# Performance work log

Measured on AMD Instinct MI355X. Metric: run time of the kernel, lower is better.

Reference implementation:

```python
import jax, jax.numpy as jnp
import numpy as np

N_TOKENS = 8192
NQ = 6
NL = 2


def ry_mat(theta):
    # theta: scalar or (B,) -> (2,2) or (B,2,2) complex RY matrix
    c = jnp.cos(theta / 2)
    s = jnp.sin(theta / 2)
    return jnp.stack([jnp.stack([c, -s], -1), jnp.stack([s, c], -1)], -2).astype(jnp.complex64)


def apply_1q(state, gate, q, nq):
    # state: (B, 2**nq); gate: (2,2) shared or (B,2,2) per-batch
    B = state.shape[0]
    st = state.reshape(B, 2 ** q, 2, -1)
    if gate.ndim == 3:
        st = jnp.einsum('bij,bajc->baic', gate, st)
    else:
        st = jnp.einsum('ij,bajc->baic', gate, st)
    return st.reshape(B, -1)


def apply_rz(state, theta, q, nq):
    # diagonal RZ: multiply phases, no matmul needed
    B = state.shape[0]
    st = state.reshape(B, 2 ** q, 2, -1)
    ph = jnp.stack([jnp.exp(-0.5j * theta), jnp.exp(0.5j * theta)]).astype(jnp.complex64)
    return (st * ph[None, None, :, None]).reshape(B, -1)


def apply_cnot(state, c, t, nq):
    B = state.shape[0]
    st = state.reshape((B,) + (2,) * nq)
    s0 = jnp.take(st, 0, axis=1 + c)
    s1 = jnp.take(st, 1, axis=1 + c)
    ta = 1 + t - (1 if t > c else 0)  # target axis after removing control axis
    s1 = jnp.flip(s1, axis=ta)
    st = jnp.stack([s0, s1], axis=1 + c)
    return st.reshape(B, -1)


def prepare_states(x, params, nl, nq):
    # x: (B, nq) angles; params: (nl, nq, 2). Returns (B, 2**nq) complex statevectors.
    B = x.shape[0]
    state = jnp.zeros((B, 2 ** nq), jnp.complex64).at[:, 0].set(1.0)
    for q in range(nq):  # RY angle embedding
        state = apply_1q(state, ry_mat(x[:, q]), q, nq)
    for l in range(nl):  # PQC layers: RY, RZ rotations + CNOT ring
        for q in range(nq):
            state = apply_1q(state, ry_mat(params[l, q, 0]), q, nq)
            state = apply_rz(state, params[l, q, 1], q, nq)
        for q in range(nq):
            state = apply_cnot(state, q, (q + 1) % nq, nq)
    return state


def setup_inputs() -> dict:
    key = jax.random.key(0)
    k1, k2, k3, k4 = jax.random.split(key, 4)
    return {
        'x_tokens': jax.random.normal(k1, (N_TOKENS, NQ), dtype=jnp.float32),
        'params_q': 0.1 * jax.random.normal(k2, (NL, NQ, 2), dtype=jnp.float32),
        'params_k': 0.1 * jax.random.normal(k3, (NL, NQ, 2), dtype=jnp.float32),
        'params_v': 0.1 * jax.random.normal(k4, (NL, NQ, 2), dtype=jnp.float32),
    }


def reference(x_tokens, params_q, params_k, params_v):
    nq = x_tokens.shape[1]
    nl = params_q.shape[0]
    sq = prepare_states(x_tokens, params_q, nl, nq)  # (N, 2**nq)
    sk = prepare_states(x_tokens, params_k, nl, nq)
    ov = jnp.einsum('id,jd->ij', sq, jnp.conj(sk))  # pairwise overlaps (N, N)
    logits = jnp.real(ov * jnp.conj(ov))            # swap-test fidelity |<q|k>|^2
    attn = jax.nn.softmax(logits, axis=-1)
    sv = prepare_states(x_tokens, params_v, nl, nq)
    probs = jnp.real(sv * jnp.conj(sv))             # (N, 2**nq)
    idx = jnp.arange(2 ** nq)
    bits = (idx[None, :] >> (nq - 1 - jnp.arange(nq))[:, None]) & 1  # (nq, 2**nq)
    signs = (1.0 - 2.0 * bits).astype(probs.dtype)
    V = probs @ signs.T                              # <Z_q> per qubit -> (N, nq)
    return attn @ V
```

## Files before the change

### kernel.cpp

```cpp
#include <hip/hip_runtime.h>
#include <hip/hip_bf16.h>

#define NT 8192
#define NQB 6
#define NL 2
#define JSPLIT 16
#define JSLICE (NT / JSPLIT)
#define CHUNK 64
#define NCHUNK (JSLICE / CHUNK)
#define IPW 32
#define WPB 4
#define IPB (IPW * WPB)
#define NBI (NT / IPB)

typedef __bf16 bf16x8 __attribute__((ext_vector_type(8)));
typedef float f32x4 __attribute__((ext_vector_type(4)));

static __device__ __forceinline__ unsigned int pack_bf2(float a, float b) {
  unsigned short lo = __builtin_bit_cast(unsigned short, __float2bfloat16(a));
  unsigned short hi = __builtin_bit_cast(unsigned short, __float2bfloat16(b));
  return (unsigned int)lo | ((unsigned int)hi << 16);
}

static __device__ __forceinline__ int cnot_src(int p, int q) {
  const int mc = 1 << (5 - q);
  const int mt = 1 << (5 - ((q + 1) % NQB));
  return (p & mc) ? (p ^ mt) : p;
}

__global__ __launch_bounds__(256) void prep_kernel(
    const float* __restrict__ x, const float* __restrict__ pq,
    const float* __restrict__ pk, const float* __restrict__ pv,
    unsigned int* __restrict__ Are, unsigned int* __restrict__ Bk,
    float4* __restrict__ V4)
{
  const int wid  = blockIdx.x * 4 + (threadIdx.x >> 6);
  const int lane = threadIdx.x & 63;
  const int set  = wid >> 13;
  const int tok  = wid & (NT - 1);
  const float* pp = (set == 0) ? pq : ((set == 1) ? pk : pv);

  int m = lane;
#pragma unroll
  for (int q = 5; q >= 0; --q) m = cnot_src(m, q);
  int inv = lane;
#pragma unroll
  for (int q = 0; q < 6; ++q) inv = cnot_src(inv, q);

  float R = 1.f, phi = 0.f;
#pragma unroll
  for (int q = 0; q < 6; ++q) {
    float s, c;
    __sincosf(0.5f * (x[tok * NQB + q] + pp[q * 2 + 0]), &s, &c);
    const float bh = 0.5f * pp[q * 2 + 1];
    if ((m >> (5 - q)) & 1) { R *= s; phi += bh; }
    else                    { R *= c; phi -= bh; }
  }
  float sp, cp;
  __sincosf(phi, &sp, &cp);
  float re = R * cp, im = R * sp;

#pragma unroll
  for (int q = 0; q < 6; ++q) {
    const int mask = 1 << (5 - q);
    float s, c;
    __sincosf(0.5f * pp[2 * NQB + q * 2 + 0], &s, &c);
    const float pre = __shfl_xor(re, mask, 64);
    const float pim = __shfl_xor(im, mask, 64);
    const float se = (lane & mask) ? s : -s;
    re = fmaf(se, pre, c * re);
    im = fmaf(se, pim, c * im);
  }
  float phi2 = 0.f;
#pragma unroll
  for (int q = 0; q < 6; ++q) {
    const float bh = 0.5f * pp[2 * NQB + q * 2 + 1];
    phi2 += (lane & (1 << (5 - q))) ? bh : -bh;
  }
  float s2, c2;
  __sincosf(phi2, &s2, &c2);
  const float fre = re * c2 - im * s2;
  const float fim = re * s2 + im * c2;

  if (set == 0) {
    Are[tok * 64 + inv] = pack_bf2(fre, fim);
  } else if (set == 1) {
    Bk[tok * 64 + inv] = pack_bf2(fre, fim);
  } else {
    const float prob = fre * fre + fim * fim;
    float vq[NQB];
#pragma unroll
    for (int q = 0; q < NQB; ++q) {
      float v = (inv & (1 << (5 - q))) ? -prob : prob;
#pragma unroll
      for (int off = 1; off < 64; off <<= 1) v += __shfl_xor(v, off, 64);
      vq[q] = v;
    }
    if (lane == 0) {
      V4[tok * 2 + 0] = make_float4(vq[0], vq[1], vq[2], vq[3]);
      V4[tok * 2 + 1] = make_float4(vq[4], vq[5], 0.f, 0.f);
    }
  }
}

__global__ __launch_bounds__(256, 2) void attn_kernel(
    const uint4* __restrict__ Are, const uint4* __restrict__ Bk,
    const float4* __restrict__ V4, float* __restrict__ part)
{
  __shared__ uint4 kbuf[CHUNK * 17];
  __shared__ float4 vbuf[CHUNK * 2];

  const int tid  = threadIdx.x;
  const int lane = tid & 63;
  const int wave = tid >> 6;
  const int col  = lane & 15;
  const int quad = lane >> 4;

  const int ib = blockIdx.x & (NBI - 1);
  const int js = blockIdx.x / NBI;
  const int ibase = ib * IPB + wave * IPW;
  const int jbase0 = js * JSLICE;

  bf16x8 aRe[2][4], aIm[2][4];
#pragma unroll
  for (int rt = 0; rt < 2; ++rt) {
    const int row = ibase + rt * 16 + col;
    const uint4* pr = Are + row * 16 + quad;
#pragma unroll
    for (int s = 0; s < 4; ++s) {
      const uint4 u = pr[s * 4];
      uint4 w;
      w.x = ((u.x << 16) | (u.x >> 16)) ^ 0x80000000u;
      w.y = ((u.y << 16) | (u.y >> 16)) ^ 0x80000000u;
      w.z = ((u.z << 16) | (u.z >> 16)) ^ 0x80000000u;
      w.w = ((u.w << 16) | (u.w >> 16)) ^ 0x80000000u;
      aRe[rt][s] = __builtin_bit_cast(bf16x8, u);
      aIm[rt][s] = __builtin_bit_cast(bf16x8, w);
    }
  }

  float den[8];
  float num[8][6];
#pragma unroll
  for (int r = 0; r < 8; ++r) {
    den[r] = 0.f;
#pragma unroll
    for (int q = 0; q < 6; ++q) num[r][q] = 0.f;
  }

#pragma unroll 1
  for (int c = 0; c < NCHUNK; ++c) {
    const int jb = jbase0 + c * CHUNK;
    __syncthreads();
#pragma unroll
    for (int r = 0; r < 4; ++r) {
      const int idx = r * 256 + tid;
      kbuf[(idx >> 4) * 17 + (idx & 15)] = Bk[(jb + (idx >> 4)) * 16 + (idx & 15)];
    }
    if (tid < 2 * CHUNK) vbuf[tid] = V4[jb * 2 + tid];
    __syncthreads();

#pragma unroll
    for (int ct = 0; ct < 4; ++ct) {
      const int keyl = ct * 16 + col;
      bf16x8 bfr[4];
#pragma unroll
      for (int s = 0; s < 4; ++s)
        bfr[s] = __builtin_bit_cast(bf16x8, kbuf[keyl * 17 + s * 4 + quad]);
      const float4 v01 = vbuf[keyl * 2 + 0];
      const float4 v23 = vbuf[keyl * 2 + 1];
      const float vv[6] = {v01.x, v01.y, v01.z, v01.w, v23.x, v23.y};
#pragma unroll
      for (int rt = 0; rt < 2; ++rt) {
        f32x4 aR = {0.f, 0.f, 0.f, 0.f};
        f32x4 aI = {0.f, 0.f, 0.f, 0.f};
#pragma unroll
        for (int s = 0; s < 4; ++s) {
          aR = __builtin_amdgcn_mfma_f32_16x16x32_bf16(aRe[rt][s], bfr[s], aR, 0, 0, 0);
          aI = __builtin_amdgcn_mfma_f32_16x16x32_bf16(aIm[rt][s], bfr[s], aI, 0, 0, 0);
        }
#pragma unroll
        for (int r = 0; r < 4; ++r) {
          const float f = aR[r] * aR[r] + aI[r] * aI[r];
          const float w = __expf(f);
          const int rr = rt * 4 + r;
          den[rr] += w;
#pragma unroll
          for (int q = 0; q < 6; ++q) num[rr][q] = fmaf(w, vv[q], num[rr][q]);
        }
      }
    }
  }

#pragma unroll
  for (int rr = 0; rr < 8; ++rr) {
#pragma unroll
    for (int off = 1; off < 16; off <<= 1) {
      den[rr] += __shfl_xor(den[rr], off, 64);
#pragma unroll
      for (int q = 0; q < 6; ++q) num[rr][q] += __shfl_xor(num[rr][q], off, 64);
    }
  }

  if (col == 0) {
#pragma unroll
    for (int rt = 0; rt < 2; ++rt) {
#pragma unroll
      for (int r = 0; r < 4; ++r) {
        const int row = ibase + rt * 16 + quad * 4 + r;
        float* p = part + ((size_t)(js * NT + row)) * 8;
        const int rr = rt * 4 + r;
#pragma unroll
        for (int q = 0; q < 6; ++q) p[q] = num[rr][q];
        p[6] = den[rr];
      }
    }
  }
}

__global__ __launch_bounds__(256) void combine_kernel(
    const float* __restrict__ part, float* __restrict__ out)
{
  const int row = blockIdx.x * 256 + threadIdx.x;
  float acc[7] = {0.f, 0.f, 0.f, 0.f, 0.f, 0.f, 0.f};
#pragma unroll
  for (int js = 0; js < JSPLIT; ++js) {
    const float* p = part + ((size_t)(js * NT + row)) * 8;
#pragma unroll
    for (int q = 0; q < 7; ++q) acc[q] += p[q];
  }
  const float inv = 1.0f / acc[6];
#pragma unroll
  for (int q = 0; q < 6; ++q)
    out[row * 6 + q] = acc[q] * inv;
}

extern "C" void kernel_launch(void* const* d_in, const int* in_sizes, int n_in,
                              void* d_out, int out_size, void* d_ws, size_t ws_size,
                              hipStream_t stream) {
  const float* x  = (const float*)d_in[0];
  const float* pq = (const float*)d_in[1];
  const float* pk = (const float*)d_in[2];
  const float* pv = (const float*)d_in[3];
  char* ws = (char*)d_ws;
  unsigned int* Are = (unsigned int*)(ws);
  unsigned int* Bk  = (unsigned int*)(ws + (size_t)(2u << 20));
  float*        V   = (float*)(ws + (size_t)(4u << 20));
  float*        prt = (float*)(ws + (size_t)(4u << 20) + (size_t)(256u << 10));

  prep_kernel<<<(NT * 3) / 4, 256, 0, stream>>>(x, pq, pk, pv, Are, Bk, (float4*)V);
  attn_kernel<<<NBI * JSPLIT, 256, 0, stream>>>((const uint4*)Are, (const uint4*)Bk,
                                                (const float4*)V, prt);
  combine_kernel<<<NT / 256, 256, 0, stream>>>(prt, (float*)d_out);
}
```

Measured before the change: 129.5 us.

## Load keys directly from global, preload V slice, restructure combine layout

The attention kernel no longer stages key chunks through shared memory with a barrier per chunk. Each wave now reads key fragments straight from global memory, relying on L1/L2 since all four waves share the same keys, and the whole V slice is preloaded once into LDS. The partial-results layout becomes row-major per js so the combine kernel can use coalesced float4 loads with 8 threads per row and a shuffle reduction. The prep kernel swaps __sincosf for separate __sinf/__cosf calls. Skipping the LDS staging risks redundant global traffic and exposed load latency in the MFMA loop.

```diff
diff --git a/kernel.cpp b/kernel.cpp
--- a/kernel.cpp
+++ b/kernel.cpp
@@ -6,12 +6,11 @@
 #define NL 2
 #define JSPLIT 16
 #define JSLICE (NT / JSPLIT)
-#define CHUNK 64
-#define NCHUNK (JSLICE / CHUNK)
 #define IPW 32
 #define WPB 4
 #define IPB (IPW * WPB)
 #define NBI (NT / IPB)
+#define NCT (JSLICE / 16)
 
 typedef __bf16 bf16x8 __attribute__((ext_vector_type(8)));
 typedef float f32x4 __attribute__((ext_vector_type(4)));
@@ -50,21 +49,19 @@
   float R = 1.f, phi = 0.f;
 #pragma unroll
   for (int q = 0; q < 6; ++q) {
-    float s, c;
-    __sincosf(0.5f * (x[tok * NQB + q] + pp[q * 2 + 0]), &s, &c);
+    const float t = 0.5f * (x[tok * NQB + q] + pp[q * 2 + 0]);
+    const float s = __sinf(t), c = __cosf(t);
     const float bh = 0.5f * pp[q * 2 + 1];
     if ((m >> (5 - q)) & 1) { R *= s; phi += bh; }
     else                    { R *= c; phi -= bh; }
   }
-  float sp, cp;
-  __sincosf(phi, &sp, &cp);
-  float re = R * cp, im = R * sp;
+  float re = R * __cosf(phi), im = R * __sinf(phi);
 
 #pragma unroll
   for (int q = 0; q < 6; ++q) {
     const int mask = 1 << (5 - q);
-    float s, c;
-    __sincosf(0.5f * pp[2 * NQB + q * 2 + 0], &s, &c);
+    const float t = 0.5f * pp[2 * NQB + q * 2 + 0];
+    const float s = __sinf(t), c = __cosf(t);
     const float pre = __shfl_xor(re, mask, 64);
     const float pim = __shfl_xor(im, mask, 64);
     const float se = (lane & mask) ? s : -s;
@@ -77,8 +74,7 @@
     const float bh = 0.5f * pp[2 * NQB + q * 2 + 1];
     phi2 += (lane & (1 << (5 - q))) ? bh : -bh;
   }
-  float s2, c2;
-  __sincosf(phi2, &s2, &c2);
+  const float s2 = __sinf(phi2), c2 = __cosf(phi2);
   const float fre = re * c2 - im * s2;
   const float fim = re * s2 + im * c2;
 
@@ -107,8 +103,7 @@
     const uint4* __restrict__ Are, const uint4* __restrict__ Bk,
     const float4* __restrict__ V4, float* __restrict__ part)
 {
-  __shared__ uint4 kbuf[CHUNK * 17];
-  __shared__ float4 vbuf[CHUNK * 2];
+  __shared__ float4 vbuf[JSLICE * 2];
 
   const int tid  = threadIdx.x;
   const int lane = tid & 63;
@@ -119,7 +114,11 @@
   const int ib = blockIdx.x & (NBI - 1);
   const int js = blockIdx.x / NBI;
   const int ibase = ib * IPB + wave * IPW;
-  const int jbase0 = js * JSLICE;
+  const int jbase = js * JSLICE;
+
+#pragma unroll
+  for (int r = 0; r < 4; ++r)
+    vbuf[r * 256 + tid] = V4[jbase * 2 + r * 256 + tid];
 
   bf16x8 aRe[2][4], aIm[2][4];
 #pragma unroll
@@ -148,46 +147,39 @@
     for (int q = 0; q < 6; ++q) num[r][q] = 0.f;
   }
 
-#pragma unroll 1
-  for (int c = 0; c < NCHUNK; ++c) {
-    const int jb = jbase0 + c * CHUNK;
-    __syncthreads();
-#pragma unroll
-    for (int r = 0; r < 4; ++r) {
-      const int idx = r * 256 + tid;
-      kbuf[(idx >> 4) * 17 + (idx & 15)] = Bk[(jb + (idx >> 4)) * 16 + (idx & 15)];
-    }
-    if (tid < 2 * CHUNK) vbuf[tid] = V4[jb * 2 + tid];
-    __syncthreads();
-
-#pragma unroll
-    for (int ct = 0; ct < 4; ++ct) {
-      const int keyl = ct * 16 + col;
-      bf16x8 bfr[4];
-#pragma unroll
-      for (int s = 0; s < 4; ++s)
-        bfr[s] = __builtin_bit_cast(bf16x8, kbuf[keyl * 17 + s * 4 + quad]);
-      const float4 v01 = vbuf[keyl * 2 + 0];
-      const float4 v23 = vbuf[keyl * 2 + 1];
-      const float vv[6] = {v01.x, v01.y, v01.z, v01.w, v23.x, v23.y};
-#pragma unroll
-      for (int rt = 0; rt < 2; ++rt) {
-        f32x4 aR = {0.f, 0.f, 0.f, 0.f};
-        f32x4 aI = {0.f, 0.f, 0.f, 0.f};
-#pragma unroll
-        for (int s = 0; s < 4; ++s) {
-          aR = __builtin_amdgcn_mfma_f32_16x16x32_bf16(aRe[rt][s], bfr[s], aR, 0, 0, 0);
-          aI = __builtin_amdgcn_mfma_f32_16x16x32_bf16(aIm[rt][s], bfr[s], aI, 0, 0, 0);
-        }
-#pragma unroll
-        for (int r = 0; r < 4; ++r) {
-          const float f = aR[r] * aR[r] + aI[r] * aI[r];
-          const float w = __expf(f);
-          const int rr = rt * 4 + r;
-          den[rr] += w;
-#pragma unroll
-          for (int q = 0; q < 6; ++q) num[rr][q] = fmaf(w, vv[q], num[rr][q]);
-        }
+  __syncthreads();
+
+#pragma unroll 2
+  for (int ct = 0; ct < NCT; ++ct) {
+    const int key  = jbase + ct * 16 + col;
+    const uint4* bp = Bk + key * 16 + quad;
+    bf16x8 bfr[4];
+#pragma unroll
+    for (int s = 0; s < 4; ++s)
+      bfr[s] = __builtin_bit_cast(bf16x8, bp[s * 4]);
+
+    const int keyl = ct * 16 + col;
+    const float4 v01 = vbuf[keyl * 2 + 0];
+    const float4 v23 = vbuf[keyl * 2 + 1];
+    const float vv[6] = {v01.x, v01.y, v01.z, v01.w, v23.x, v23.y};
+
+#pragma unroll
+    for (int rt = 0; rt < 2; ++rt) {
+      f32x4 aR = {0.f, 0.f, 0.f, 0.f};
+      f32x4 aI = {0.f, 0.f, 0.f, 0.f};
+#pragma unroll
+      for (int s = 0; s < 4; ++s) {
+        aR = __builtin_amdgcn_mfma_f32_16x16x32_bf16(aRe[rt][s], bfr[s], aR, 0, 0, 0);
+        aI = __builtin_amdgcn_mfma_f32_16x16x32_bf16(aIm[rt][s], bfr[s], aI, 0, 0, 0);
+      }
+#pragma unroll
+      for (int r = 0; r < 4; ++r) {
+        const float f = aR[r] * aR[r] + aI[r] * aI[r];
+        const float w = __expf(f);
+        const int rr = rt * 4 + r;
+        den[rr] += w;
+#pragma unroll
+        for (int q = 0; q < 6; ++q) num[rr][q] = fmaf(w, vv[q], num[rr][q]);
       }
     }
   }
@@ -208,7 +200,7 @@
 #pragma unroll
       for (int r = 0; r < 4; ++r) {
         const int row = ibase + rt * 16 + quad * 4 + r;
-        float* p = part + ((size_t)(js * NT + row)) * 8;
+        float* p = part + ((size_t)(row * JSPLIT + js)) * 8;
         const int rr = rt * 4 + r;
 #pragma unroll
         for (int q = 0; q < 6; ++q) p[q] = num[rr][q];
@@ -219,20 +211,31 @@
 }
 
 __global__ __launch_bounds__(256) void combine_kernel(
-    const float* __restrict__ part, float* __restrict__ out)
+    const float4* __restrict__ part4, float* __restrict__ out)
 {
-  const int row = blockIdx.x * 256 + threadIdx.x;
+  const int tid = threadIdx.x;
+  const int row = blockIdx.x * 32 + (tid >> 3);
+  const int sub = tid & 7;
+
   float acc[7] = {0.f, 0.f, 0.f, 0.f, 0.f, 0.f, 0.f};
 #pragma unroll
-  for (int js = 0; js < JSPLIT; ++js) {
-    const float* p = part + ((size_t)(js * NT + row)) * 8;
-#pragma unroll
-    for (int q = 0; q < 7; ++q) acc[q] += p[q];
-  }
-  const float inv = 1.0f / acc[6];
-#pragma unroll
-  for (int q = 0; q < 6; ++q)
-    out[row * 6 + q] = acc[q] * inv;
+  for (int h = 0; h < 2; ++h) {
+    const int js = sub + h * 8;
+    const float4 a0 = part4[(row * JSPLIT + js) * 2 + 0];
+    const float4 a1 = part4[(row * JSPLIT + js) * 2 + 1];
+    acc[0] += a0.x; acc[1] += a0.y; acc[2] += a0.z; acc[3] += a0.w;
+    acc[4] += a1.x; acc[5] += a1.y; acc[6] += a1.z;
+  }
+#pragma unroll
+  for (int off = 1; off < 8; off <<= 1) {
+#pragma unroll
+    for (int q = 0; q < 7; ++q) acc[q] += __shfl_xor(acc[q], off, 64);
+  }
+  if (sub == 0) {
+    const float inv = 1.0f / acc[6];
+#pragma unroll
+    for (int q = 0; q < 6; ++q) out[row * 6 + q] = acc[q] * inv;
+  }
 }
 
 extern "C" void kernel_launch(void* const* d_in, const int* in_sizes, int n_in,
@@ -251,5 +254,5 @@
   prep_kernel<<<(NT * 3) / 4, 256, 0, stream>>>(x, pq, pk, pv, Are, Bk, (float4*)V);
   attn_kernel<<<NBI * JSPLIT, 256, 0, stream>>>((const uint4*)Are, (const uint4*)Bk,
                                                 (const float4*)V, prt);
-  combine_kernel<<<NT / 256, 256, 0, stream>>>(prt, (float*)d_out);
-}
+  combine_kernel<<<NT / 32, 256, 0, stream>>>((const float4*)prt, (float*)d_out);
+}
```

Measured after the change: 146.6 us. 13.1% more time.
